# Performance work log

Hardware: AMD Instinct MI355X
Metric: run time of the kernel (lower is better)

The kernel has to match this reference:

```python
import jax, jax.numpy as jnp
import numpy as np

E = 23   # unique experts
K = 3    # active experts per token

def setup_inputs() -> dict:
    key = jax.random.key(0)
    ks = jax.random.split(key, 11)
    d, h, B, N = 1024, 768, 16, 196
    s = 0.02  # init scale so sigmoid gate is non-saturated
    return {
        "x":      jax.random.normal(ks[0], (B, N, d), jnp.float32),
        "gate_w": jax.random.normal(ks[1], (d, E), jnp.float32) * s,
        "gate_b": jnp.zeros((E,), jnp.float32),
        "w1":     jax.random.normal(ks[2], (E, d, h), jnp.float32) * s,
        "b1":     jnp.zeros((E, h), jnp.float32),
        "w2":     jax.random.normal(ks[3], (E, h, d), jnp.float32) * s,
        "b2":     jnp.zeros((E, d), jnp.float32),
        "ws1":    jax.random.normal(ks[4], (d, h), jnp.float32) * s,
        "bs1":    jnp.zeros((h,), jnp.float32),
        "ws2":    jax.random.normal(ks[5], (h, d), jnp.float32) * s,
        "bs2":    jnp.zeros((d,), jnp.float32),
    }

def reference(x, gate_w, gate_b, w1, b1, w2, b2, ws1, bs1, ws2, bs2):
    o_shape = x.shape
    xt = x.reshape(-1, o_shape[-1])            # [T, d]
    T = xt.shape[0]

    # gating: sigmoid gate, top-3 (the 'bias' buffer in the source is zeros)
    gw = jax.nn.sigmoid(xt @ gate_w + gate_b)  # [T, E]
    top_vals, top_idx = jax.lax.top_k(gw, K)   # [T, K]
    tw = top_vals / top_vals.sum(-1, keepdims=True)

    # dense combine weights: tw scattered to [T, E] (0 for unselected experts)
    w_dense = jnp.zeros_like(gw).at[jnp.arange(T)[:, None], top_idx].add(tw)

    # expert MLPs (dense-masked equivalent of the grouped dispatch)
    hh = jax.nn.gelu(jnp.einsum('td,edh->teh', xt, w1) + b1, approximate=False)
    eo = jnp.einsum('teh,ehd->ted', hh, w2) + b2          # [T, E, d]

    # shared expert
    shared = jax.nn.gelu(xt @ ws1 + bs1, approximate=False) @ ws2 + bs2

    out = shared + jnp.einsum('ted,te->td', eo, w_dense)  # [T, d]

    # aux load-balancing loss
    gwn = gw / gw.sum(-1, keepdims=True)
    P = gwn.mean(0)                                       # [E]
    counts = jnp.zeros((E,), gw.dtype).at[top_idx.reshape(-1)].add(1.0)
    Fv = E * counts / (K * T)
    aux = (P * Fv).sum()

    return out.reshape(o_shape), aux
```

## Files before the change

kernel.cpp:

```cpp
#include <hip/hip_runtime.h>
#include <hip/hip_bf16.h>

#define T_TOK 3136
#define DDIM  1024
#define HDIM  768
#define NEXP  23
#define TOPK  3
#define MTILE 128
#define NTILE 128
#define KTILE 32
#define LDSB  40
#define MAXTILES 128
#define MAX_SLOTS 16384
#define GATE_BLOCKS 1568
#define XCVT_BLOCKS 3136

typedef __attribute__((ext_vector_type(8))) short  short8;
typedef __attribute__((ext_vector_type(4))) short  short4v;
typedef __attribute__((ext_vector_type(4))) float  floatx4;

__device__ __forceinline__ short f2b(float f) {
    union { float f; unsigned u; } v; v.f = f;
    unsigned r = v.u + 0x7FFFu + ((v.u >> 16) & 1u);
    return (short)(r >> 16);
}
__device__ __forceinline__ float b2f(short s) {
    union { unsigned u; float f; } v; v.u = ((unsigned)(unsigned short)s) << 16; return v.f;
}
__device__ __forceinline__ float gelu_exact(float v) {
    return 0.5f * v * (1.0f + erff(v * 0.70710678118654752f));
}
__device__ __forceinline__ void gld16(const short* g, short* l) {
    __builtin_amdgcn_global_load_lds(
        (const __attribute__((address_space(1))) void*)g,
        (__attribute__((address_space(3))) void*)l, 16, 0, 0);
}

__global__ __launch_bounds__(256) void prep_kernel(
    const float* __restrict__ x, short* __restrict__ xb,
    const float* __restrict__ gw, float* __restrict__ gwT)
{
    __shared__ float tile[32][33];
    if (blockIdx.x < XCVT_BLOCKS) {
        int i = blockIdx.x * 256 + threadIdx.x;
        float4 v = ((const float4*)x)[i];
        short4v s = { f2b(v.x), f2b(v.y), f2b(v.z), f2b(v.w) };
        ((short4v*)xb)[i] = s;
        return;
    }
    const int kt = blockIdx.x - XCVT_BLOCKS;
    const int tx = threadIdx.x & 31, ty = threadIdx.x >> 5;
    #pragma unroll
    for (int i = 0; i < 4; i++) {
        int k = ty + i * 8;
        tile[k][tx] = (tx < NEXP) ? gw[(size_t)(kt * 32 + k) * NEXP + tx] : 0.f;
    }
    __syncthreads();
    #pragma unroll
    for (int i = 0; i < 4; i++) {
        int e = ty + i * 8;
        if (e < 24) gwT[(size_t)e * DDIM + kt * 32 + tx] = tile[tx][e];
    }
}

__global__ __launch_bounds__(256) void gate_kernel(
    const float* __restrict__ x, const float* __restrict__ gwT, const float* __restrict__ gb,
    float* __restrict__ Pf, int* __restrict__ top_idx, float* __restrict__ top_w)
{
    const int tid = threadIdx.x;
    const int lane = tid & 63, wave = tid >> 6;
    const int ebase = wave * 6;
    __shared__ float sg[24];
    __shared__ float accP[NEXP];
    if (tid < NEXP) accP[tid] = 0.f;

    for (int t = blockIdx.x; t < T_TOK; t += GATE_BLOCKS) {
        const float4* xr4 = (const float4*)(x + (size_t)t * DDIM);
        float4 xv[4];
        #pragma unroll
        for (int j = 0; j < 4; j++) xv[j] = xr4[j * 64 + lane];

        double a0 = 0, a1 = 0, a2 = 0, a3 = 0, a4 = 0, a5 = 0;
        #pragma unroll
        for (int j = 0; j < 4; j++) {
            const float4* gp = (const float4*)gwT + (size_t)ebase * 256 + j * 64 + lane;
            float4 g0 = gp[0 * 256], g1 = gp[1 * 256], g2 = gp[2 * 256];
            float4 g3 = gp[3 * 256], g4 = gp[4 * 256], g5 = gp[5 * 256];
            float4 xj = xv[j];
            a0 += (double)xj.x * g0.x + (double)xj.y * g0.y + (double)xj.z * g0.z + (double)xj.w * g0.w;
            a1 += (double)xj.x * g1.x + (double)xj.y * g1.y + (double)xj.z * g1.z + (double)xj.w * g1.w;
            a2 += (double)xj.x * g2.x + (double)xj.y * g2.y + (double)xj.z * g2.z + (double)xj.w * g2.w;
            a3 += (double)xj.x * g3.x + (double)xj.y * g3.y + (double)xj.z * g3.z + (double)xj.w * g3.w;
            a4 += (double)xj.x * g4.x + (double)xj.y * g4.y + (double)xj.z * g4.z + (double)xj.w * g4.w;
            a5 += (double)xj.x * g5.x + (double)xj.y * g5.y + (double)xj.z * g5.z + (double)xj.w * g5.w;
        }
        #pragma unroll
        for (int off = 32; off > 0; off >>= 1) {
            a0 += __shfl_xor(a0, off);
            a1 += __shfl_xor(a1, off);
            a2 += __shfl_xor(a2, off);
            a3 += __shfl_xor(a3, off);
            a4 += __shfl_xor(a4, off);
            a5 += __shfl_xor(a5, off);
        }

        if (lane == 0) {
            double av[6] = { a0, a1, a2, a3, a4, a5 };
            #pragma unroll
            for (int i = 0; i < 6; i++) {
                int e = ebase + i;
                if (e < NEXP) {
                    float z = (float)av[i] + gb[e];
                    sg[e] = 1.0f / (1.0f + expf(-z));
                }
            }
        }
        __syncthreads();

        if (tid < NEXP) {
            float s = 0.f;
            #pragma unroll
            for (int e = 0; e < NEXP; e++) s += sg[e];
            accP[tid] += sg[tid] / s;
        }
        if (tid == 0) {
            float v0 = -1.f, v1 = -1.f, v2 = -1.f; int i0 = 0, i1 = 0, i2 = 0;
            for (int e = 0; e < NEXP; e++) {
                float v = sg[e];
                if (v > v0)      { v2 = v1; i2 = i1; v1 = v0; i1 = i0; v0 = v; i0 = e; }
                else if (v > v1) { v2 = v1; i2 = i1; v1 = v; i1 = e; }
                else if (v > v2) { v2 = v; i2 = e; }
            }
            float ts = v0 + v1 + v2;
            top_idx[t * 3 + 0] = i0; top_w[t * 3 + 0] = v0 / ts;
            top_idx[t * 3 + 1] = i1; top_w[t * 3 + 1] = v1 / ts;
            top_idx[t * 3 + 2] = i2; top_w[t * 3 + 2] = v2 / ts;
        }
        __syncthreads();
    }
    if (tid < NEXP) atomicAdd(&Pf[tid], accP[tid]);
}

__global__ __launch_bounds__(1024) void route_kernel(
    const int* __restrict__ top_idx, const float* __restrict__ Pf,
    int* __restrict__ ntl,
    int* __restrict__ slot_t, int* __restrict__ slot_of,
    int* __restrict__ tmap_e, int* __restrict__ tmap_b,
    float* __restrict__ out_aux)
{
    __shared__ int h[NEXP];
    __shared__ int lfill[NEXP];
    __shared__ int soffs[NEXP + 1];
    __shared__ int sntl[NEXP + 1];
    const int tid = threadIdx.x;
    if (tid < NEXP) { h[tid] = 0; lfill[tid] = 0; }
    __syncthreads();
    for (int i = tid; i < T_TOK * 3; i += 1024) atomicAdd(&h[top_idx[i]], 1);
    __syncthreads();
    if (tid == 0) {
        int o = 0, ti = 0;
        for (int e = 0; e < NEXP; e++) {
            int c = h[e];
            int nt = (c + MTILE - 1) / MTILE;
            soffs[e] = o; sntl[e] = nt; ntl[e] = nt;
            for (int j = 0; j < nt; j++) { tmap_e[ti] = e; tmap_b[ti] = o + j * MTILE; ti++; }
            o += nt * MTILE;
        }
        int nts = (T_TOK + MTILE - 1) / MTILE;
        soffs[NEXP] = o; sntl[NEXP] = nts; ntl[NEXP] = nts;
        for (int j = 0; j < nts; j++) { tmap_e[ti] = NEXP; tmap_b[ti] = o + j * MTILE; ti++; }
        ntl[NEXP + 1] = ti;
        float aux = 0.f;
        for (int e = 0; e < NEXP; e++) {
            float P = Pf[e] / (float)T_TOK;
            float F = (float)NEXP * (float)h[e] / (float)(TOPK * T_TOK);
            aux += P * F;
        }
        out_aux[0] = aux;
    }
    __syncthreads();
    for (int e = 0; e <= NEXP; e++) {
        int cnt = (e < NEXP) ? h[e] : T_TOK;
        int s0 = soffs[e] + cnt, s1 = soffs[e] + sntl[e] * MTILE;
        for (int s = s0 + tid; s < s1; s += 1024) slot_t[s] = 0;
    }
    for (int t = tid; t < T_TOK; t += 1024) {
        #pragma unroll
        for (int k = 0; k < TOPK; k++) {
            int e = top_idx[t * 3 + k];
            int pos = atomicAdd(&lfill[e], 1);
            int s = soffs[e] + pos;
            slot_t[s] = t;
            slot_of[t * 4 + k] = s;
        }
        int s = soffs[NEXP] + t;
        slot_t[s] = t;
        slot_of[t * 4 + 3] = s;
    }
}

__global__ __launch_bounds__(256) void gemm1_kernel(
    const short* __restrict__ xb,
    const float* __restrict__ w1, const float* __restrict__ b1,
    const float* __restrict__ ws1, const float* __restrict__ bs1,
    const int* __restrict__ tmap_e, const int* __restrict__ tmap_b,
    const int* __restrict__ ntl,
    const int* __restrict__ slot_t, short* __restrict__ hh)
{
    const int L = blockIdx.x;
    const int xcd = L & 7, sl = L >> 3;
    const int ty = xcd * 16 + sl / 6, tx = sl % 6;
    if (ty >= ntl[NEXP + 1]) return;
    const int e = tmap_e[ty];
    const int slot_base = tmap_b[ty];
    const int n0 = tx * NTILE;
    const float* __restrict__ Wf = (e < NEXP) ? (w1 + (size_t)e * DDIM * HDIM) : ws1;
    const float* __restrict__ Bv = (e < NEXP) ? (b1 + (size_t)e * HDIM) : bs1;

    __shared__ __align__(16) short As[2][MTILE * KTILE];
    __shared__ __align__(16) short Bs[2][NTILE * LDSB];
    __shared__ int toks[MTILE];

    const int tid = threadIdx.x;
    for (int i = tid; i < MTILE; i += 256) toks[i] = slot_t[slot_base + i];

    const int lane = tid & 63, wave = tid >> 6;
    const int mbase = (wave & 1) * 64, nbase = (wave >> 1) * 64;
    const int lc = lane & 15, q = lane >> 4;
    const int xq8 = (q ^ ((lc >> 1) & 3)) << 3;

    const int srow = wave * 16 + (lane >> 2);
    const int c8   = (lane & 3) * 8;

    __syncthreads();
    const short* gA0 = xb + (size_t)toks[srow]      * DDIM + c8;
    const short* gA1 = xb + (size_t)toks[64 + srow] * DDIM + c8;
    const int lofs0 = wave * 512, lofs1 = 2048 + wave * 512;

    const int g = wave, cn = lane;
    const float* gW = Wf + (size_t)(8 * g) * HDIM + n0 + 2 * cn;
    const int bws = (g ^ (cn & 3)) << 3;
    const int bofs0 = (2 * cn) * LDSB + bws, bofs1 = (2 * cn + 1) * LDSB + bws;

    floatx4 acc[4][4];
    #pragma unroll
    for (int m = 0; m < 4; m++)
        #pragma unroll
        for (int n = 0; n < 4; n++) acc[m][n] = (floatx4)0.f;

    const int NT = DDIM / KTILE;
    float2 f[8];
    #pragma unroll
    for (int j = 0; j < 8; j++) f[j] = *(const float2*)(gW + (size_t)j * HDIM);
    gld16(gA0, &As[0][lofs0]);
    gld16(gA1, &As[0][lofs1]);
    {
        short8 s0, s1;
        #pragma unroll
        for (int j = 0; j < 8; j++) { s0[j] = f2b(f[j].x); s1[j] = f2b(f[j].y); }
        *(short8*)&Bs[0][bofs0] = s0;
        *(short8*)&Bs[0][bofs1] = s1;
    }
    #pragma unroll
    for (int j = 0; j < 8; j++) f[j] = *(const float2*)(gW + (size_t)(KTILE + j) * HDIM);
    __syncthreads();

    for (int t = 0; t < NT; t++) {
        const int cur = t & 1;
        if (t + 1 < NT) {
            gld16(gA0 + (t + 1) * KTILE, &As[cur ^ 1][lofs0]);
            gld16(gA1 + (t + 1) * KTILE, &As[cur ^ 1][lofs1]);
            short8 s0, s1;
            #pragma unroll
            for (int j = 0; j < 8; j++) { s0[j] = f2b(f[j].x); s1[j] = f2b(f[j].y); }
            *(short8*)&Bs[cur ^ 1][bofs0] = s0;
            *(short8*)&Bs[cur ^ 1][bofs1] = s1;
        }
        if (t + 2 < NT) {
            #pragma unroll
            for (int j = 0; j < 8; j++)
                f[j] = *(const float2*)(gW + (size_t)((t + 2) * KTILE + j) * HDIM);
        }
        short8 af[4], bf[4];
        #pragma unroll
        for (int m = 0; m < 4; m++) af[m] = *(const short8*)&As[cur][(mbase + m * 16 + lc) * KTILE + q * 8];
        #pragma unroll
        for (int n = 0; n < 4; n++) bf[n] = *(const short8*)&Bs[cur][(nbase + n * 16 + lc) * LDSB + xq8];
        #pragma unroll
        for (int m = 0; m < 4; m++)
            #pragma unroll
            for (int n = 0; n < 4; n++)
                acc[m][n] = __builtin_amdgcn_mfma_f32_16x16x32_bf16(af[m], bf[n], acc[m][n], 0, 0, 0);
        __syncthreads();
    }

    #pragma unroll
    for (int n = 0; n < 4; n++) {
        const int col = n0 + nbase + n * 16 + lc;
        const float bb = Bv[col];
        #pragma unroll
        for (int m = 0; m < 4; m++) {
            const int rbase = slot_base + mbase + m * 16 + q * 4;
            #pragma unroll
            for (int r = 0; r < 4; r++) {
                float v = acc[m][n][r] + bb;
                hh[(size_t)(rbase + r) * HDIM + col] = f2b(gelu_exact(v));
            }
        }
    }
}

__global__ __launch_bounds__(256) void gemm2_kernel(
    const short* __restrict__ hh,
    const float* __restrict__ w2, const float* __restrict__ b2,
    const float* __restrict__ ws2, const float* __restrict__ bs2,
    const int* __restrict__ tmap_e, const int* __restrict__ tmap_b,
    const int* __restrict__ ntl,
    short* __restrict__ eo)
{
    const int L = blockIdx.x;
    const int xcd = L & 7, sl = L >> 3;
    const int ty = xcd * 16 + sl / 8, tx = sl & 7;
    if (ty >= ntl[NEXP + 1]) return;
    const int e = tmap_e[ty];
    const int slot_base = tmap_b[ty];
    const int n0 = tx * NTILE;
    const float* __restrict__ Wf = (e < NEXP) ? (w2 + (size_t)e * HDIM * DDIM) : ws2;
    const float* __restrict__ Bv = (e < NEXP) ? (b2 + (size_t)e * DDIM) : bs2;

    __shared__ __align__(16) short As[2][MTILE * KTILE];
    __shared__ __align__(16) short Bs[2][NTILE * LDSB];

    const int tid = threadIdx.x;
    const int lane = tid & 63, wave = tid >> 6;
    const int mbase = (wave & 1) * 64, nbase = (wave >> 1) * 64;
    const int lc = lane & 15, q = lane >> 4;
    const int xq8 = (q ^ ((lc >> 1) & 3)) << 3;

    const int srow = wave * 16 + (lane >> 2);
    const int c8   = (lane & 3) * 8;

    const short* gA0 = hh + (size_t)(slot_base + srow)      * HDIM + c8;
    const short* gA1 = hh + (size_t)(slot_base + 64 + srow) * HDIM + c8;
    const int lofs0 = wave * 512, lofs1 = 2048 + wave * 512;

    const int g = wave, cn = lane;
    const float* gW = Wf + (size_t)(8 * g) * DDIM + n0 + 2 * cn;
    const int bws = (g ^ (cn & 3)) << 3;
    const int bofs0 = (2 * cn) * LDSB + bws, bofs1 = (2 * cn + 1) * LDSB + bws;

    floatx4 acc[4][4];
    #pragma unroll
    for (int m = 0; m < 4; m++)
        #pragma unroll
        for (int n = 0; n < 4; n++) acc[m][n] = (floatx4)0.f;

    const int NT = HDIM / KTILE;
    float2 f[8];
    #pragma unroll
    for (int j = 0; j < 8; j++) f[j] = *(const float2*)(gW + (size_t)j * DDIM);
    gld16(gA0, &As[0][lofs0]);
    gld16(gA1, &As[0][lofs1]);
    {
        short8 s0, s1;
        #pragma unroll
        for (int j = 0; j < 8; j++) { s0[j] = f2b(f[j].x); s1[j] = f2b(f[j].y); }
        *(short8*)&Bs[0][bofs0] = s0;
        *(short8*)&Bs[0][bofs1] = s1;
    }
    #pragma unroll
    for (int j = 0; j < 8; j++) f[j] = *(const float2*)(gW + (size_t)(KTILE + j) * DDIM);
    __syncthreads();

    for (int t = 0; t < NT; t++) {
        const int cur = t & 1;
        if (t + 1 < NT) {
            gld16(gA0 + (t + 1) * KTILE, &As[cur ^ 1][lofs0]);
            gld16(gA1 + (t + 1) * KTILE, &As[cur ^ 1][lofs1]);
            short8 s0, s1;
            #pragma unroll
            for (int j = 0; j < 8; j++) { s0[j] = f2b(f[j].x); s1[j] = f2b(f[j].y); }
            *(short8*)&Bs[cur ^ 1][bofs0] = s0;
            *(short8*)&Bs[cur ^ 1][bofs1] = s1;
        }
        if (t + 2 < NT) {
            #pragma unroll
            for (int j = 0; j < 8; j++)
                f[j] = *(const float2*)(gW + (size_t)((t + 2) * KTILE + j) * DDIM);
        }
        short8 af[4], bf[4];
        #pragma unroll
        for (int m = 0; m < 4; m++) af[m] = *(const short8*)&As[cur][(mbase + m * 16 + lc) * KTILE + q * 8];
        #pragma unroll
        for (int n = 0; n < 4; n++) bf[n] = *(const short8*)&Bs[cur][(nbase + n * 16 + lc) * LDSB + xq8];
        #pragma unroll
        for (int m = 0; m < 4; m++)
            #pragma unroll
            for (int n = 0; n < 4; n++)
                acc[m][n] = __builtin_amdgcn_mfma_f32_16x16x32_bf16(af[m], bf[n], acc[m][n], 0, 0, 0);
        __syncthreads();
    }

    #pragma unroll
    for (int n = 0; n < 4; n++) {
        const int col = n0 + nbase + n * 16 + lc;
        const float bb = Bv[col];
        #pragma unroll
        for (int m = 0; m < 4; m++) {
            const int rbase = slot_base + mbase + m * 16 + q * 4;
            #pragma unroll
            for (int r = 0; r < 4; r++)
                eo[(size_t)(rbase + r) * DDIM + col] = f2b(acc[m][n][r] + bb);
        }
    }
}

__global__ __launch_bounds__(256) void combine_kernel(
    const short* __restrict__ eo, const float* __restrict__ top_w,
    const int* __restrict__ slot_of, float* __restrict__ out)
{
    const int t = blockIdx.x;
    const int c = threadIdx.x * 4;
    const int s0 = slot_of[t * 4 + 0], s1 = slot_of[t * 4 + 1];
    const int s2 = slot_of[t * 4 + 2], s3 = slot_of[t * 4 + 3];
    const float w0 = top_w[t * 3 + 0], w1 = top_w[t * 3 + 1], w2 = top_w[t * 3 + 2];
    short4v a = *(const short4v*)(eo + (size_t)s0 * DDIM + c);
    short4v b = *(const short4v*)(eo + (size_t)s1 * DDIM + c);
    short4v d = *(const short4v*)(eo + (size_t)s2 * DDIM + c);
    short4v s = *(const short4v*)(eo + (size_t)s3 * DDIM + c);
    float4 o;
    o.x = b2f(s.x) + w0 * b2f(a.x) + w1 * b2f(b.x) + w2 * b2f(d.x);
    o.y = b2f(s.y) + w0 * b2f(a.y) + w1 * b2f(b.y) + w2 * b2f(d.y);
    o.z = b2f(s.z) + w0 * b2f(a.z) + w1 * b2f(b.z) + w2 * b2f(d.z);
    o.w = b2f(s.w) + w0 * b2f(a.w) + w1 * b2f(b.w) + w2 * b2f(d.w);
    *(float4*)(out + (size_t)t * DDIM + c) = o;
}

extern "C" void kernel_launch(void* const* d_in, const int* in_sizes, int n_in,
                              void* d_out, int out_size, void* d_ws, size_t ws_size,
                              hipStream_t stream)
{
    const float* x   = (const float*)d_in[0];
    const float* gw  = (const float*)d_in[1];
    const float* gb  = (const float*)d_in[2];
    const float* w1  = (const float*)d_in[3];
    const float* b1  = (const float*)d_in[4];
    const float* w2  = (const float*)d_in[5];
    const float* b2  = (const float*)d_in[6];
    const float* ws1 = (const float*)d_in[7];
    const float* bs1 = (const float*)d_in[8];
    const float* ws2 = (const float*)d_in[9];
    const float* bs2 = (const float*)d_in[10];
    float* out = (float*)d_out;

    char* p = (char*)d_ws;
    auto alloc = [&](size_t bytes) -> char* {
        char* r = p; p += (bytes + 255) & ~(size_t)255; return r;
    };
    int*   top_idx  = (int*)  alloc((size_t)T_TOK * 3 * 4);
    float* top_w    = (float*)alloc((size_t)T_TOK * 3 * 4);
    float* Pf       = (float*)alloc(NEXP * 4);
    int*   ntl      = (int*)  alloc((NEXP + 2) * 4);
    int*   slot_t   = (int*)  alloc((size_t)MAX_SLOTS * 4);
    int*   slot_of  = (int*)  alloc((size_t)T_TOK * 4 * 4);
    int*   tmap_e   = (int*)  alloc((size_t)MAXTILES * 4);
    int*   tmap_b   = (int*)  alloc((size_t)MAXTILES * 4);
    float* gwT      = (float*)alloc((size_t)24 * DDIM * 4);
    short* xb       = (short*)alloc((size_t)T_TOK * DDIM * 2);
    short* hh       = (short*)alloc((size_t)MAX_SLOTS * HDIM * 2);
    short* eo       = (short*)alloc((size_t)MAX_SLOTS * DDIM * 2);

    hipMemsetAsync(Pf, 0, NEXP * 4, stream);

    prep_kernel<<<XCVT_BLOCKS + DDIM / 32, 256, 0, stream>>>(x, xb, gw, gwT);
    gate_kernel<<<GATE_BLOCKS, 256, 0, stream>>>(x, gwT, gb, Pf, top_idx, top_w);
    route_kernel<<<1, 1024, 0, stream>>>(top_idx, Pf, ntl, slot_t, slot_of,
                                         tmap_e, tmap_b, out + (size_t)T_TOK * DDIM);
    gemm1_kernel<<<8 * 16 * 6, 256, 0, stream>>>(
        xb, w1, b1, ws1, bs1, tmap_e, tmap_b, ntl, slot_t, hh);
    gemm2_kernel<<<8 * 16 * 8, 256, 0, stream>>>(
        hh, w2, b2, ws2, bs2, tmap_e, tmap_b, ntl, eo);
    combine_kernel<<<T_TOK, 256, 0, stream>>>(eo, top_w, slot_of, out);
}
```

Before: 389.7 us.

## Replace GEMM syncthreads with partial vmcnt waits and drop Pf memset

In both grouped GEMM kernels, the per-iteration __syncthreads is replaced by a barrier that waits only until the current tile's global loads have landed (vmcnt(8)), leaving the next tile's eight weight prefetch loads in flight. Scheduling barriers pin the load issue order so the counter-based wait stays valid, and the barrier after the final iteration is skipped. The separate hipMemsetAsync of Pf is folded into prep_kernel, removing one launch. The vmcnt arithmetic depends on the exact instruction order the compiler emits, so a miscount could produce races.

```diff
diff --git a/kernel.cpp b/kernel.cpp
--- a/kernel.cpp
+++ b/kernel.cpp
@@ -35,13 +35,24 @@
         (const __attribute__((address_space(1))) void*)g,
         (__attribute__((address_space(3))) void*)l, 16, 0, 0);
 }
+__device__ __forceinline__ void bar_cnt8() {
+    asm volatile("s_waitcnt vmcnt(8) lgkmcnt(0)" ::: "memory");
+    __builtin_amdgcn_s_barrier();
+    __builtin_amdgcn_sched_barrier(0);
+}
+__device__ __forceinline__ void bar_cnt0() {
+    asm volatile("s_waitcnt vmcnt(0) lgkmcnt(0)" ::: "memory");
+    __builtin_amdgcn_s_barrier();
+    __builtin_amdgcn_sched_barrier(0);
+}
 
 __global__ __launch_bounds__(256) void prep_kernel(
     const float* __restrict__ x, short* __restrict__ xb,
-    const float* __restrict__ gw, float* __restrict__ gwT)
+    const float* __restrict__ gw, float* __restrict__ gwT, float* __restrict__ Pf)
 {
     __shared__ float tile[32][33];
     if (blockIdx.x < XCVT_BLOCKS) {
+        if (blockIdx.x == 0 && threadIdx.x < NEXP) Pf[threadIdx.x] = 0.f;
         int i = blockIdx.x * 256 + threadIdx.x;
         float4 v = ((const float4*)x)[i];
         short4v s = { f2b(v.x), f2b(v.y), f2b(v.z), f2b(v.w) };
@@ -254,6 +265,7 @@
     for (int j = 0; j < 8; j++) f[j] = *(const float2*)(gW + (size_t)j * HDIM);
     gld16(gA0, &As[0][lofs0]);
     gld16(gA1, &As[0][lofs1]);
+    __builtin_amdgcn_sched_barrier(0);
     {
         short8 s0, s1;
         #pragma unroll
@@ -263,13 +275,14 @@
     }
     #pragma unroll
     for (int j = 0; j < 8; j++) f[j] = *(const float2*)(gW + (size_t)(KTILE + j) * HDIM);
-    __syncthreads();
+    bar_cnt8();
 
     for (int t = 0; t < NT; t++) {
         const int cur = t & 1;
         if (t + 1 < NT) {
             gld16(gA0 + (t + 1) * KTILE, &As[cur ^ 1][lofs0]);
             gld16(gA1 + (t + 1) * KTILE, &As[cur ^ 1][lofs1]);
+            __builtin_amdgcn_sched_barrier(0);
             short8 s0, s1;
             #pragma unroll
             for (int j = 0; j < 8; j++) { s0[j] = f2b(f[j].x); s1[j] = f2b(f[j].y); }
@@ -291,7 +304,10 @@
             #pragma unroll
             for (int n = 0; n < 4; n++)
                 acc[m][n] = __builtin_amdgcn_mfma_f32_16x16x32_bf16(af[m], bf[n], acc[m][n], 0, 0, 0);
-        __syncthreads();
+        if (t + 1 < NT) {
+            if (t + 2 < NT) bar_cnt8();
+            else            bar_cnt0();
+        }
     }
 
     #pragma unroll
@@ -361,6 +377,7 @@
     for (int j = 0; j < 8; j++) f[j] = *(const float2*)(gW + (size_t)j * DDIM);
     gld16(gA0, &As[0][lofs0]);
     gld16(gA1, &As[0][lofs1]);
+    __builtin_amdgcn_sched_barrier(0);
     {
         short8 s0, s1;
         #pragma unroll
@@ -370,13 +387,14 @@
     }
     #pragma unroll
     for (int j = 0; j < 8; j++) f[j] = *(const float2*)(gW + (size_t)(KTILE + j) * DDIM);
-    __syncthreads();
+    bar_cnt8();
 
     for (int t = 0; t < NT; t++) {
         const int cur = t & 1;
         if (t + 1 < NT) {
             gld16(gA0 + (t + 1) * KTILE, &As[cur ^ 1][lofs0]);
             gld16(gA1 + (t + 1) * KTILE, &As[cur ^ 1][lofs1]);
+            __builtin_amdgcn_sched_barrier(0);
             short8 s0, s1;
             #pragma unroll
             for (int j = 0; j < 8; j++) { s0[j] = f2b(f[j].x); s1[j] = f2b(f[j].y); }
@@ -398,7 +416,10 @@
             #pragma unroll
             for (int n = 0; n < 4; n++)
                 acc[m][n] = __builtin_amdgcn_mfma_f32_16x16x32_bf16(af[m], bf[n], acc[m][n], 0, 0, 0);
-        __syncthreads();
+        if (t + 1 < NT) {
+            if (t + 2 < NT) bar_cnt8();
+            else            bar_cnt0();
+        }
     }
 
     #pragma unroll
@@ -470,9 +491,7 @@
     short* hh       = (short*)alloc((size_t)MAX_SLOTS * HDIM * 2);
     short* eo       = (short*)alloc((size_t)MAX_SLOTS * DDIM * 2);
 
-    hipMemsetAsync(Pf, 0, NEXP * 4, stream);
-
-    prep_kernel<<<XCVT_BLOCKS + DDIM / 32, 256, 0, stream>>>(x, xb, gw, gwT);
+    prep_kernel<<<XCVT_BLOCKS + DDIM / 32, 256, 0, stream>>>(x, xb, gw, gwT, Pf);
     gate_kernel<<<GATE_BLOCKS, 256, 0, stream>>>(x, gwT, gb, Pf, top_idx, top_w);
     route_kernel<<<1, 1024, 0, stream>>>(top_idx, Pf, ntl, slot_t, slot_of,
                                          tmap_e, tmap_b, out + (size_t)T_TOK * DDIM);
```

After: 380.0 us. 1.03x faster.
